# Optimization experiments

Measured on AMD Instinct MI355X. Metric: run time of the kernel, lower is better.

The kernel has to match this reference:

```python
import jax, jax.numpy as jnp
import numpy as np

EMBED = 512; HEADS = 16; WIN = 8; SHIFT = 4

def _rel_pos_index(Wh, Ww):
    # WindowMSA.double_step_seq + transpose-sum + flip(1)
    seq1 = np.arange(0, (2 * Ww - 1) * Wh, 2 * Ww - 1)
    seq2 = np.arange(0, Ww)
    coords = (seq1[:, None] + seq2[None, :]).reshape(1, -1)
    idx = coords + coords.T            # (Wh*Ww, Wh*Ww)
    return idx[:, ::-1].copy()

def _attn_mask(H_pad, W_pad, win, shift, nf):
    # static (trace-time) shifted-window mask, values in {0, -100}
    img = np.zeros((H_pad, W_pad))
    cnt = 0
    for h in (slice(0, -win), slice(-win, -shift), slice(-shift, None)):
        for w in (slice(0, -win), slice(-win, -shift), slice(-shift, None)):
            img[h, w] = cnt
            cnt += 1
    mw = img.reshape(H_pad // win, win, W_pad // win, win).transpose(0, 2, 1, 3).reshape(-1, win * win)
    am = mw[:, None, :] - mw[:, :, None]
    am = np.where(am != 0, -100.0, 0.0)
    return np.tile(am, (1, 1, nf))     # (nW, N, nf*N)

def setup_inputs():
    key = jax.random.key(0)
    ks = jax.random.split(key, 8)
    B, H, W, C, nf = 8, 128, 128, EMBED, 2
    s = 0.02
    return {
        'q': jax.random.normal(ks[0], (B, H * W, C), jnp.float32),
        'kv': jax.random.normal(ks[1], (B, nf, H * W, C), jnp.float32),
        'H': H, 'W': W,
        'rpb_table': jax.random.normal(ks[2], ((2 * WIN - 1) ** 2, HEADS), jnp.float32) * s,
        'Wq': jax.random.normal(ks[3], (C, C), jnp.float32) * s,
        'bq': jnp.zeros((C,), jnp.float32),
        'Wkv': jax.random.normal(ks[4], (C, 2 * C), jnp.float32) * s,
        'bkv': jnp.zeros((2 * C,), jnp.float32),
        'Wo': jax.random.normal(ks[5], (C, C), jnp.float32) * s,
        'bo': jnp.zeros((C,), jnp.float32),
    }

def reference(q, kv, H, W, rpb_table, Wq, bq, Wkv, bkv, Wo, bo):
    B, L, C = q.shape
    nf = kv.shape[1]
    win, shift, heads = WIN, SHIFT, HEADS
    hd = C // heads
    scale = hd ** -0.5
    pad_b = (-H) % win
    pad_r = (-W) % win
    x = q.reshape(B, H, W, C)
    kvx = kv.reshape(B * nf, H, W, C)
    x = jnp.pad(x, ((0, 0), (0, pad_b), (0, pad_r), (0, 0)))
    kvx = jnp.pad(kvx, ((0, 0), (0, pad_b), (0, pad_r), (0, 0)))
    Hp, Wp = H + pad_b, W + pad_r
    nh, nw = Hp // win, Wp // win
    if shift > 0:
        x = jnp.roll(x, (-shift, -shift), (1, 2))
        kvx = jnp.roll(kvx, (-shift, -shift), (1, 2))
        mask = jnp.asarray(_attn_mask(Hp, Wp, win, shift, nf), q.dtype)
    else:
        mask = None
    Nq = win * win
    Nk = nf * Nq
    # window partition: (B, Hp, Wp, C) -> (B*nh*nw, Nq, C)
    qw = x.reshape(B, nh, win, nw, win, C).transpose(0, 1, 3, 2, 4, 5).reshape(B * nh * nw, Nq, C)
    # kv: (B*nf, Hp, Wp, C) -> (B*nh*nw, nf*Nq, C)
    kvw = kvx.reshape(B, nf, nh, win, nw, win, C).transpose(0, 2, 4, 1, 3, 5, 6).reshape(B * nh * nw, Nk, C)
    Bw = qw.shape[0]
    qh = (qw @ Wq + bq).reshape(Bw, Nq, heads, hd).transpose(0, 2, 1, 3) * scale
    kvp = (kvw @ Wkv + bkv).reshape(Bw, Nk, 2, heads, hd).transpose(2, 0, 3, 1, 4)
    kh, vh = kvp[0], kvp[1]
    attn = jnp.einsum('bhqd,bhkd->bhqk', qh, kh)
    rpi = jnp.asarray(_rel_pos_index(win, win).reshape(-1))
    rpb = rpb_table[rpi].reshape(Nq, Nq, heads).transpose(2, 0, 1)  # (heads, Nq, Nq)
    attn = attn + jnp.tile(rpb, (1, 1, nf))[None]
    if mask is not None:
        nW = mask.shape[0]
        attn = (attn.reshape(Bw // nW, nW, heads, Nq, Nk) + mask[None, :, None]).reshape(Bw, heads, Nq, Nk)
    attn = jax.nn.softmax(attn, axis=-1)
    ow = jnp.einsum('bhqk,bhkd->bqhd', attn, vh).reshape(Bw, Nq, C)
    ow = ow @ Wo + bo
    # window reverse
    x = ow.reshape(B, nh, nw, win, win, C).transpose(0, 1, 3, 2, 4, 5).reshape(B, Hp, Wp, C)
    if shift > 0:
        x = jnp.roll(x, (shift, shift), (1, 2))
    x = x[:, :H, :W, :].reshape(B, H * W, C)
    return x
```

## Files before the change

### kernel.cpp

```cpp
#include <hip/hip_runtime.h>

typedef unsigned short ushort_t;
typedef short bf16x8 __attribute__((ext_vector_type(8)));
typedef float f32x4 __attribute__((ext_vector_type(4)));

#define MFMA16(a, b, c) __builtin_amdgcn_mfma_f32_16x16x32_bf16(a, b, c, 0, 0, 0)

static __device__ __forceinline__ float bf2f(ushort_t u) {
  union { unsigned int i; float f; } v;
  v.i = ((unsigned int)u) << 16;
  return v.f;
}
static __device__ __forceinline__ ushort_t f2bf(float f) {
  union { float f; unsigned int i; } v;
  v.f = f;
  unsigned int u = v.i;
  u = u + 0x7fffu + ((u >> 16) & 1u);
  return (ushort_t)(u >> 16);
}
static __device__ __forceinline__ unsigned int cvtpk(float lo, float hi) {
  unsigned int r;
  asm("v_cvt_pk_bf16_f32 %0, %1, %2" : "=v"(r) : "v"(lo), "v"(hi));
  return r;
}
static __device__ __forceinline__ void gload16(const void* g, void* l) {
  __builtin_amdgcn_global_load_lds((const __attribute__((address_space(1))) void*)g,
                                   (__attribute__((address_space(3))) void*)l,
                                   16, 0, 0);
}

__global__ void ws_sentinel(float* out, unsigned long long ws) {
  if (blockIdx.x == 0 && threadIdx.x == 0)
    out[0] = 1.0e6f * (1.0f + (float)(ws >> 23));
}

__global__ __launch_bounds__(256) void wtrans3(const float* __restrict__ Wq,
                                               const float* __restrict__ Wkv,
                                               const float* __restrict__ Wo,
                                               ushort_t* __restrict__ WqT,
                                               ushort_t* __restrict__ WkvT,
                                               ushort_t* __restrict__ WoT) {
  int idx = blockIdx.x * 256 + threadIdx.x;
  if (idx < 262144) {
    int r = idx >> 9, c = idx & 511;
    WqT[c * 512 + r] = f2bf(Wq[idx]);
  } else if (idx < 786432) {
    int i = idx - 262144;
    int r = i >> 10, c = i & 1023;
    WkvT[c * 512 + r] = f2bf(Wkv[i]);
  } else if (idx < 1048576) {
    int i = idx - 786432;
    int r = i >> 9, c = i & 511;
    WoT[c * 512 + r] = f2bf(Wo[i]);
  }
}

template <bool AF32, bool CF32>
__global__ __launch_bounds__(512, 2) void gemm_bt(const void* __restrict__ Av,
                                                  const ushort_t* __restrict__ Bt,
                                                  const float* __restrict__ bias,
                                                  void* __restrict__ Cv,
                                                  int N, int Nt) {
  constexpr int K = 512;
  __shared__ __align__(16) unsigned char As[AF32 ? 128 * 32 * 4 : 128 * 32 * 2];
  __shared__ __align__(16) unsigned char Bs[256 * 32 * 2];
  const int t = threadIdx.x;
  const int l = t & 63;
  const int w = t >> 6;
  const int wr = w >> 2, wc = w & 3;
  const int lrow = l & 15;
  const int g = l >> 4;

  const int bid = blockIdx.x;
  const int xcd = bid & 7;
  const int slot = bid >> 3;
  const int mt = xcd + 8 * (slot / Nt);
  const int nt = slot % Nt;
  const long m0 = (long)mt * 128;
  const int n0 = nt * 256;

  const int arow = l >> 3;
  const int acol = ((16 * (l & 7)) ^ ((arow & 7) << 4)) >> 2;
  const int brow = l >> 2;
  const int bcol = ((16 * (l & 3)) ^ ((brow & 3) << 4)) >> 1;

  const f32x4 fz = {0.f, 0.f, 0.f, 0.f};
  f32x4 acc[4][4];
#pragma unroll
  for (int i = 0; i < 4; i++)
#pragma unroll
    for (int j = 0; j < 4; j++) acc[i][j] = fz;

  for (int kk = 0; kk < K; kk += 32) {
    __syncthreads();
    if constexpr (AF32) {
#pragma unroll
      for (int i = 0; i < 2; i++) {
        const float* gp = (const float*)Av + (m0 + w * 16 + i * 8 + arow) * (long)K + kk + acol;
        gload16(gp, &As[(w * 16 + i * 8) * 128]);
      }
    } else {
      const ushort_t* gp = (const ushort_t*)Av + (m0 + w * 16 + brow) * (long)K + kk + bcol;
      gload16(gp, &As[(w * 16) * 64]);
    }
#pragma unroll
    for (int i = 0; i < 2; i++) {
      const ushort_t* gp = Bt + (long)(n0 + w * 32 + i * 16 + brow) * K + kk + bcol;
      gload16(gp, &Bs[(w * 32 + i * 16) * 64]);
    }
    __syncthreads();

    bf16x8 af[4], bfr[4];
    if constexpr (AF32) {
#pragma unroll
      for (int mi = 0; mi < 4; mi++) {
        const int aR = wr * 64 + mi * 16 + lrow;
        const int s = (aR & 7) << 4;
        const int c0 = g * 32;
        f32x4 x = *(const f32x4*)&As[aR * 128 + (c0 ^ s)];
        f32x4 y = *(const f32x4*)&As[aR * 128 + ((c0 + 16) ^ s)];
        union { unsigned int u[4]; bf16x8 v; } r;
        r.u[0] = cvtpk(x[0], x[1]);
        r.u[1] = cvtpk(x[2], x[3]);
        r.u[2] = cvtpk(y[0], y[1]);
        r.u[3] = cvtpk(y[2], y[3]);
        af[mi] = r.v;
      }
    } else {
#pragma unroll
      for (int mi = 0; mi < 4; mi++) {
        const int aR = wr * 64 + mi * 16 + lrow;
        af[mi] = *(const bf16x8*)&As[aR * 64 + ((g * 16) ^ ((aR & 3) << 4))];
      }
    }
#pragma unroll
    for (int ni = 0; ni < 4; ni++) {
      const int bR = wc * 64 + ni * 16 + lrow;
      bfr[ni] = *(const bf16x8*)&Bs[bR * 64 + ((g * 16) ^ ((bR & 3) << 4))];
    }
#pragma unroll
    for (int mi = 0; mi < 4; mi++)
#pragma unroll
      for (int ni = 0; ni < 4; ni++)
        acc[mi][ni] = MFMA16(af[mi], bfr[ni], acc[mi][ni]);
  }

#pragma unroll
  for (int mi = 0; mi < 4; mi++) {
    const long row0 = m0 + wr * 64 + mi * 16 + (l >> 4) * 4;
#pragma unroll
    for (int ni = 0; ni < 4; ni++) {
      const int col = n0 + wc * 64 + ni * 16 + lrow;
      const float bv = bias[col];
#pragma unroll
      for (int r = 0; r < 4; r++) {
        const float val = acc[mi][ni][r] + bv;
        if constexpr (CF32)
          ((float*)Cv)[(row0 + r) * N + col] = val;
        else
          ((ushort_t*)Cv)[(row0 + r) * N + col] = f2bf(val);
      }
    }
  }
}

__global__ __launch_bounds__(256, 1) void attn_k(const ushort_t* __restrict__ Qp,
                                                 const ushort_t* __restrict__ KVp,
                                                 const float* __restrict__ rpbt,
                                                 ushort_t* __restrict__ Ao) {
  __shared__ ushort_t P[64 * 136];
  __shared__ __align__(16) unsigned char poolKV[32 * 136 * 2];
  __shared__ float Ltab[225];
  ushort_t* Ks = (ushort_t*)poolKV;
  ushort_t* Vt = (ushort_t*)poolKV;
  const int t = threadIdx.x;
  const int l = t & 63;
  const int w = t >> 6;
  const int wnd = blockIdx.x;
  const int h = blockIdx.y;
  const int b = wnd >> 8;
  const int wh = (wnd >> 4) & 15;
  const int ww = wnd & 15;

  const int lrow = l & 15;
  const int lq = l >> 4;
  const int lk = lq * 8;

  auto qrow = [&](int q) -> long {
    int i = q >> 3, j = q & 7;
    int ho = (wh * 8 + i + 4) & 127;
    int wo = (ww * 8 + j + 4) & 127;
    return (long)((b << 14) + (ho << 7) + wo);
  };
  auto kvrow = [&](int kp) -> long {
    int f = kp >> 6, m = kp & 63;
    int i = m >> 3, j = m & 7;
    int ho = (wh * 8 + i + 4) & 127;
    int wo = (ww * 8 + j + 4) & 127;
    return (long)(((b * 2 + f) << 14) + (ho << 7) + wo);
  };
  auto cnt_of = [&](int m) -> int {
    int hr = wh * 8 + (m >> 3), wr2 = ww * 8 + (m & 7);
    int rh = hr < 120 ? 0 : (hr < 124 ? 1 : 2);
    int rw = wr2 < 120 ? 0 : (wr2 < 124 ? 1 : 2);
    return rh * 3 + rw;
  };
  auto cvec = [](int m) -> int { return 15 * (m >> 3) + (m & 7); };

#pragma unroll
  for (int i = 0; i < 2; i++) {
    const int row = w * 32 + i * 16 + (l >> 2);
    const ushort_t* gp = KVp + kvrow(row) * 1024 + h * 32 + (l & 3) * 8;
    gload16(gp, Ks + (w * 32 + i * 16) * 32);
  }
  for (int i = t; i < 225; i += 256) Ltab[i] = rpbt[i * 16 + h];

  bf16x8 af = *(const bf16x8*)(Qp + qrow(w * 16 + lrow) * 512 + h * 32 + lk);

  __syncthreads();

  const f32x4 fz = {0.f, 0.f, 0.f, 0.f};
  f32x4 s[8];
#pragma unroll
  for (int ni = 0; ni < 8; ni++) s[ni] = fz;
#pragma unroll
  for (int ni = 0; ni < 8; ni++) {
    bf16x8 kf = *(const bf16x8*)&Ks[(ni * 16 + lrow) * 32 + lk];
    s[ni] = MFMA16(af, kf, s[ni]);
  }

  const float scale = 0.17677669529663687f;
#pragma unroll
  for (int r = 0; r < 4; r++) {
    const int q = w * 16 + lq * 4 + r;
    const int cq = cnt_of(q);
    const int cqv = cvec(q);
    float mx = -3.0e38f;
#pragma unroll
    for (int ni = 0; ni < 8; ni++) {
      const int k63 = (ni * 16 + lrow) & 63;
      float v = s[ni][r] * scale + Ltab[cqv + cvec(63 - k63)];
      if (cnt_of(k63) != cq) v -= 100.f;
      s[ni][r] = v;
      mx = fmaxf(mx, v);
    }
    mx = fmaxf(mx, __shfl_xor(mx, 1));
    mx = fmaxf(mx, __shfl_xor(mx, 2));
    mx = fmaxf(mx, __shfl_xor(mx, 4));
    mx = fmaxf(mx, __shfl_xor(mx, 8));
    float sum = 0.f;
#pragma unroll
    for (int ni = 0; ni < 8; ni++) {
      float p = __expf(s[ni][r] - mx);
      s[ni][r] = p;
      sum += p;
    }
    sum += __shfl_xor(sum, 1);
    sum += __shfl_xor(sum, 2);
    sum += __shfl_xor(sum, 4);
    sum += __shfl_xor(sum, 8);
    const float inv = 1.f / sum;
#pragma unroll
    for (int ni = 0; ni < 8; ni++)
      P[q * 136 + ni * 16 + lrow] = f2bf(s[ni][r] * inv);
  }

  __syncthreads();

  {
    const int kp = t & 127;
    const int dh = t >> 7;
    const ushort_t* src = KVp + kvrow(kp) * 1024 + 512 + h * 32 + dh * 16;
    bf16x8 v0 = *(const bf16x8*)(src);
    bf16x8 v1 = *(const bf16x8*)(src + 8);
#pragma unroll
    for (int d = 0; d < 8; d++) {
      Vt[(dh * 16 + d) * 136 + kp] = (ushort_t)v0[d];
      Vt[(dh * 16 + 8 + d) * 136 + kp] = (ushort_t)v1[d];
    }
  }
  __syncthreads();

  f32x4 o[2] = {fz, fz};
#pragma unroll
  for (int ks = 0; ks < 4; ks++) {
    bf16x8 pf = *(const bf16x8*)&P[(w * 16 + lrow) * 136 + ks * 32 + lk];
#pragma unroll
    for (int ni = 0; ni < 2; ni++) {
      bf16x8 vf = *(const bf16x8*)&Vt[(ni * 16 + lrow) * 136 + ks * 32 + lk];
      o[ni] = MFMA16(pf, vf, o[ni]);
    }
  }

#pragma unroll
  for (int ni = 0; ni < 2; ni++)
#pragma unroll
    for (int r = 0; r < 4; r++) {
      const int q = w * 16 + lq * 4 + r;
      Ao[qrow(q) * 512 + h * 32 + ni * 16 + lrow] = f2bf(o[ni][r]);
    }
}

extern "C" void kernel_launch(void* const* d_in, const int* in_sizes, int n_in,
                              void* d_out, int out_size, void* d_ws, size_t ws_size,
                              hipStream_t stream) {
  (void)in_sizes; (void)n_in; (void)out_size;
  const float* q    = (const float*)d_in[0];
  const float* kv   = (const float*)d_in[1];
  const float* rpbt = (const float*)d_in[4];
  const float* Wq   = (const float*)d_in[5];
  const float* bq   = (const float*)d_in[6];
  const float* Wkv  = (const float*)d_in[7];
  const float* bkv  = (const float*)d_in[8];
  const float* Wo   = (const float*)d_in[9];
  const float* bo   = (const float*)d_in[10];
  float* out = (float*)d_out;

  const size_t QB  = 16384ULL * 512;
  const size_t KVB = 32768ULL * 1024;
  const size_t per_b_bytes = (QB + QB + KVB) * 2;
  const size_t fixed_bytes = (512ULL*512 + 512ULL*1024 + 512ULL*512) * 2;
  const size_t needed1 = fixed_bytes + per_b_bytes;

  if (ws_size < needed1) {
    ws_sentinel<<<dim3(1), 64, 0, stream>>>(out, (unsigned long long)ws_size);
    return;
  }

  int nbc = 8;
  while (nbc > 1 && fixed_bytes + (size_t)nbc * per_b_bytes > ws_size) nbc >>= 1;

  char* ws = (char*)d_ws;
  ushort_t* WqT  = (ushort_t*)ws;
  ushort_t* WkvT = WqT + 512 * 512;
  ushort_t* WoT  = WkvT + 512 * 1024;
  ushort_t* Qp   = (ushort_t*)(ws + fixed_bytes);
  ushort_t* Ao   = Qp + (size_t)nbc * QB;
  ushort_t* KVp  = Ao + (size_t)nbc * QB;

  wtrans3<<<dim3(4096), 256, 0, stream>>>(Wq, Wkv, Wo, WqT, WkvT, WoT);

  for (int c = 0; c < 8 / nbc; ++c) {
    const size_t b0 = (size_t)c * nbc;
    const int MtQ = nbc * 128;
    const int MtKV = nbc * 256;
    gemm_bt<true, false><<<dim3(MtQ * 2), 512, 0, stream>>>(q + b0 * QB, WqT, bq,
                                                            Qp, 512, 2);
    gemm_bt<true, false><<<dim3(MtKV * 4), 512, 0, stream>>>(kv + b0 * KVB / 2, WkvT,
                                                             bkv, KVp, 1024, 4);
    attn_k<<<dim3(nbc * 256, 16), 256, 0, stream>>>(Qp, KVp, rpbt, Ao);
    gemm_bt<false, true><<<dim3(MtQ * 2), 512, 0, stream>>>(Ao, WoT, bo,
                                                            out + b0 * QB, 512, 2);
  }
}
```

Before: 1.054 ms.

## Double-buffer GEMM LDS tiles and shrink block to 128x128 with 4 waves

The projection GEMM now uses two LDS buffers and prefetches the K-tile two steps ahead, with explicit vmcnt waits and barriers, so global loads overlap MFMA work. The block tile also changes from 128x256 with 8 waves to 128x128 with 4 waves, which doubles the grid and halves the N-tile size. The aim is to hide global memory latency in the K loop. The cost is more LDS per block, fewer threads per block, and more redundant A-tile loads across blocks.

```diff
diff --git a/kernel.cpp b/kernel.cpp
--- a/kernel.cpp
+++ b/kernel.cpp
@@ -56,18 +56,21 @@
 }
 
 template <bool AF32, bool CF32>
-__global__ __launch_bounds__(512, 2) void gemm_bt(const void* __restrict__ Av,
+__global__ __launch_bounds__(256, 2) void gemm_bt(const void* __restrict__ Av,
                                                   const ushort_t* __restrict__ Bt,
                                                   const float* __restrict__ bias,
                                                   void* __restrict__ Cv,
                                                   int N, int Nt) {
   constexpr int K = 512;
-  __shared__ __align__(16) unsigned char As[AF32 ? 128 * 32 * 4 : 128 * 32 * 2];
-  __shared__ __align__(16) unsigned char Bs[256 * 32 * 2];
+  constexpr int NT = K / 32;
+  constexpr int ABYTES = AF32 ? 128 * 32 * 4 : 128 * 32 * 2;
+  __shared__ __align__(16) unsigned char As[2][ABYTES];
+  __shared__ __align__(16) unsigned char Bs[2][128 * 32 * 2];
   const int t = threadIdx.x;
   const int l = t & 63;
   const int w = t >> 6;
-  const int wr = w >> 2, wc = w & 3;
+  const int w32 = w * 32;
+  const int wr = w >> 1, wc = w & 1;
   const int lrow = l & 15;
   const int g = l >> 4;
 
@@ -77,13 +80,34 @@
   const int mt = xcd + 8 * (slot / Nt);
   const int nt = slot % Nt;
   const long m0 = (long)mt * 128;
-  const int n0 = nt * 256;
+  const int n0 = nt * 128;
 
   const int arow = l >> 3;
   const int acol = ((16 * (l & 7)) ^ ((arow & 7) << 4)) >> 2;
   const int brow = l >> 2;
   const int bcol = ((16 * (l & 3)) ^ ((brow & 3) << 4)) >> 1;
 
+  auto stage = [&](int buf, int kk) {
+    if constexpr (AF32) {
+#pragma unroll
+      for (int i = 0; i < 4; i++) {
+        const float* gp = (const float*)Av + (m0 + w32 + i * 8 + arow) * (long)K + kk + acol;
+        gload16(gp, &As[buf][(w32 + i * 8) * 128]);
+      }
+    } else {
+#pragma unroll
+      for (int i = 0; i < 2; i++) {
+        const ushort_t* gp = (const ushort_t*)Av + (m0 + w32 + i * 16 + brow) * (long)K + kk + bcol;
+        gload16(gp, &As[buf][(w32 + i * 16) * 64]);
+      }
+    }
+#pragma unroll
+    for (int i = 0; i < 2; i++) {
+      const ushort_t* gp = Bt + (long)(n0 + w32 + i * 16 + brow) * K + kk + bcol;
+      gload16(gp, &Bs[buf][(w32 + i * 16) * 64]);
+    }
+  };
+
   const f32x4 fz = {0.f, 0.f, 0.f, 0.f};
   f32x4 acc[4][4];
 #pragma unroll
@@ -91,24 +115,21 @@
 #pragma unroll
     for (int j = 0; j < 4; j++) acc[i][j] = fz;
 
-  for (int kk = 0; kk < K; kk += 32) {
-    __syncthreads();
-    if constexpr (AF32) {
-#pragma unroll
-      for (int i = 0; i < 2; i++) {
-        const float* gp = (const float*)Av + (m0 + w * 16 + i * 8 + arow) * (long)K + kk + acol;
-        gload16(gp, &As[(w * 16 + i * 8) * 128]);
-      }
+  stage(0, 0);
+  stage(1, 32);
+
+#pragma unroll
+  for (int ts = 0; ts < NT; ++ts) {
+    const int cur = ts & 1;
+    if (ts < NT - 1) {
+      if constexpr (AF32) asm volatile("s_waitcnt vmcnt(6)" ::: "memory");
+      else                asm volatile("s_waitcnt vmcnt(4)" ::: "memory");
     } else {
-      const ushort_t* gp = (const ushort_t*)Av + (m0 + w * 16 + brow) * (long)K + kk + bcol;
-      gload16(gp, &As[(w * 16) * 64]);
-    }
-#pragma unroll
-    for (int i = 0; i < 2; i++) {
-      const ushort_t* gp = Bt + (long)(n0 + w * 32 + i * 16 + brow) * K + kk + bcol;
-      gload16(gp, &Bs[(w * 32 + i * 16) * 64]);
-    }
-    __syncthreads();
+      asm volatile("s_waitcnt vmcnt(0)" ::: "memory");
+    }
+    __builtin_amdgcn_sched_barrier(0);
+    __builtin_amdgcn_s_barrier();
+    __builtin_amdgcn_sched_barrier(0);
 
     bf16x8 af[4], bfr[4];
     if constexpr (AF32) {
@@ -117,8 +138,8 @@
         const int aR = wr * 64 + mi * 16 + lrow;
         const int s = (aR & 7) << 4;
         const int c0 = g * 32;
-        f32x4 x = *(const f32x4*)&As[aR * 128 + (c0 ^ s)];
-        f32x4 y = *(const f32x4*)&As[aR * 128 + ((c0 + 16) ^ s)];
+        f32x4 x = *(const f32x4*)&As[cur][aR * 128 + (c0 ^ s)];
+        f32x4 y = *(const f32x4*)&As[cur][aR * 128 + ((c0 + 16) ^ s)];
         union { unsigned int u[4]; bf16x8 v; } r;
         r.u[0] = cvtpk(x[0], x[1]);
         r.u[1] = cvtpk(x[2], x[3]);
@@ -130,19 +151,25 @@
 #pragma unroll
       for (int mi = 0; mi < 4; mi++) {
         const int aR = wr * 64 + mi * 16 + lrow;
-        af[mi] = *(const bf16x8*)&As[aR * 64 + ((g * 16) ^ ((aR & 3) << 4))];
+        af[mi] = *(const bf16x8*)&As[cur][aR * 64 + ((g * 16) ^ ((aR & 3) << 4))];
       }
     }
 #pragma unroll
     for (int ni = 0; ni < 4; ni++) {
       const int bR = wc * 64 + ni * 16 + lrow;
-      bfr[ni] = *(const bf16x8*)&Bs[bR * 64 + ((g * 16) ^ ((bR & 3) << 4))];
+      bfr[ni] = *(const bf16x8*)&Bs[cur][bR * 64 + ((g * 16) ^ ((bR & 3) << 4))];
     }
 #pragma unroll
     for (int mi = 0; mi < 4; mi++)
 #pragma unroll
       for (int ni = 0; ni < 4; ni++)
         acc[mi][ni] = MFMA16(af[mi], bfr[ni], acc[mi][ni]);
+
+    __builtin_amdgcn_sched_barrier(0);
+    __builtin_amdgcn_s_barrier();
+    __builtin_amdgcn_sched_barrier(0);
+    asm volatile("" ::: "memory");
+    if (ts + 2 < NT) stage(cur, (ts + 2) * 32);
   }
 
 #pragma unroll
@@ -344,12 +371,12 @@
     const size_t b0 = (size_t)c * nbc;
     const int MtQ = nbc * 128;
     const int MtKV = nbc * 256;
-    gemm_bt<true, false><<<dim3(MtQ * 2), 512, 0, stream>>>(q + b0 * QB, WqT, bq,
-                                                            Qp, 512, 2);
-    gemm_bt<true, false><<<dim3(MtKV * 4), 512, 0, stream>>>(kv + b0 * KVB / 2, WkvT,
-                                                             bkv, KVp, 1024, 4);
+    gemm_bt<true, false><<<dim3(MtQ * 4), 256, 0, stream>>>(q + b0 * QB, WqT, bq,
+                                                            Qp, 512, 4);
+    gemm_bt<true, false><<<dim3(MtKV * 8), 256, 0, stream>>>(kv + b0 * KVB / 2, WkvT,
+                                                             bkv, KVp, 1024, 8);
     attn_k<<<dim3(nbc * 256, 16), 256, 0, stream>>>(Qp, KVp, rpbt, Ao);
-    gemm_bt<false, true><<<dim3(MtQ * 2), 512, 0, stream>>>(Ao, WoT, bo,
-                                                            out + b0 * QB, 512, 2);
-  }
-}
+    gemm_bt<false, true><<<dim3(MtQ * 4), 256, 0, stream>>>(Ao, WoT, bo,
+                                                            out + b0 * QB, 512, 4);
+  }
+}
```

After: 1.063 ms. About the same (+0.9%).
